# Kernel optimization log

Measured on AMD Instinct MI355X. Metric: run time of the kernel, lower is better.

The kernel has to match this reference:

```python
import jax, jax.numpy as jnp
import numpy as np
from jax import lax

CHUNK = 64
D_CONV = 4
EPS = 1e-5


def _rmsnorm(x, w):
    ms = jnp.mean(jnp.square(x.astype(jnp.float32)), axis=-1, keepdims=True)
    return x * lax.rsqrt(ms + EPS).astype(x.dtype) * w


def _conv_mix(x, proj_w, gate_w, conv_w, conv_b, out_proj_w):
    # x: [B,L,D] -> depthwise causal conv on projected channels, silu gate, out proj
    B, L, D = x.shape
    val = jnp.einsum('bld,ed->ble', x, proj_w)            # [B,L,d_inner]
    v = val.transpose(0, 2, 1)                            # [B,d_inner,L]
    d_inner = proj_w.shape[0]
    v = lax.conv_general_dilated(
        v, conv_w, window_strides=(1,), padding=[(D_CONV - 1, 0)],
        dimension_numbers=('NCH', 'OIH', 'NCH'), feature_group_count=d_inner)
    v = v + conv_b[None, :, None]
    val = jax.nn.silu(v.transpose(0, 2, 1))               # [B,L,d_inner]
    gate = jax.nn.silu(jnp.einsum('bld,ed->ble', x, gate_w))
    return jnp.einsum('ble,de->bld', val * gate, out_proj_w)


def _memory_attend(out, write_w, read_w, decay, log_alpha):
    B, T, D = out.shape
    C = CHUNK
    out32 = out.astype(jnp.float32)
    gamma = jax.nn.sigmoid(decay)
    log_gamma = jnp.log(gamma)
    v = jnp.einsum('btd,ed->bte', out32, write_w)         # proj_write
    wk = jnp.pad(out32[:, :-1], ((0, 0), (1, 0), (0, 0)))  # shifted keys
    rk = out32
    p = jnp.arange(C, dtype=jnp.float32)
    gp = gamma ** p                                       # [C]
    gw = gamma ** (C - 1 - p)                              # [C]
    diffs = jnp.maximum(p[:, None] - 1.0 - p[None, :], 0.0)
    M = jnp.exp(diffs * log_gamma) * (p[:, None] > p[None, :])  # [C,C]
    gC = gamma ** C
    Nc = T // C
    # scan axis first: [Nc,B,C,D]
    rk_c = rk.reshape(B, Nc, C, D).transpose(1, 0, 2, 3)
    wk_c = wk.reshape(B, Nc, C, D).transpose(1, 0, 2, 3)
    v_c = v.reshape(B, Nc, C, D).transpose(1, 0, 2, 3)

    def step(W, chunk):
        r, k, vv = chunk                                  # each [B,C,D]
        inter = jnp.einsum('bcd,bed->bce', r, W) * gp[None, :, None]
        S = jnp.einsum('bcd,bed->bce', r, k)              # [B,C,C]
        intra = jnp.einsum('bce,bed->bcd', S * M, vv)
        W_new = gC * W + jnp.einsum('bcd,bce->bde', vv * gw[None, :, None], k)
        return W_new, inter + intra

    W0 = jnp.zeros((B, D, D), dtype=jnp.float32)
    _, reads = lax.scan(step, W0, (rk_c, wk_c, v_c))      # [Nc,B,C,D]
    reads = reads.transpose(1, 0, 2, 3).reshape(B, T, D)
    read_out = jnp.einsum('btd,ed->bte', reads, read_w)
    return out + jnp.exp(log_alpha) * read_out.astype(out.dtype)


def setup_inputs() -> dict:
    key = jax.random.key(0)
    ks = jax.random.split(key, 9)
    B, T, D, d_inner = 8, 4096, 768, 1536
    s_d = 1.0 / np.sqrt(D)
    s_i = 1.0 / np.sqrt(d_inner)
    return {
        'x': jax.random.normal(ks[0], (B, T, D), jnp.float32),
        'norm_w': jnp.ones((D,), jnp.float32),
        'proj_w': jax.random.normal(ks[1], (d_inner, D), jnp.float32) * s_d,
        'gate_w': jax.random.normal(ks[2], (d_inner, D), jnp.float32) * s_d,
        'conv_w': jax.random.normal(ks[3], (d_inner, 1, D_CONV), jnp.float32) * 0.5,
        'conv_b': jnp.zeros((d_inner,), jnp.float32),
        'out_proj_w': jax.random.normal(ks[4], (D, d_inner), jnp.float32) * s_i,
        'write_w': jax.random.normal(ks[5], (D, D), jnp.float32) * s_d,
        'read_w': jax.random.normal(ks[6], (D, D), jnp.float32) * s_d,
        'decay': jnp.float32(4.6),
        'log_alpha': jnp.log(jnp.float32(0.03)),
    }


def reference(x, norm_w, proj_w, gate_w, conv_w, conv_b, out_proj_w, write_w, read_w, decay, log_alpha):
    out = _conv_mix(_rmsnorm(x, norm_w), proj_w, gate_w, conv_w, conv_b, out_proj_w)
    out = _memory_attend(out, write_w, read_w, decay, log_alpha)
    return x + out
```

## Files before the change

kernel.cpp:

```cpp
#include <hip/hip_runtime.h>
#include <stdint.h>


typedef short bf16s;
typedef __attribute__((ext_vector_type(8))) short short8;
typedef __attribute__((ext_vector_type(4))) float f32x4;

#define DEVINL __device__ __forceinline__

DEVINL float bf2f(short s) {
    union { unsigned u; float f; } v; v.u = ((unsigned)(unsigned short)s) << 16; return v.f;
}
DEVINL short f2bf(float f) {
    union { float f; unsigned u; } v; v.f = f;
    unsigned r = v.u + 0x7fffu + ((v.u >> 16) & 1u);
    return (short)(r >> 16);
}

DEVINL void glds16(void* lds, const void* g) {
    __builtin_amdgcn_global_load_lds(
        (const __attribute__((address_space(1))) void*)g,
        (__attribute__((address_space(3))) void*)lds, 16, 0, 0);
}

DEVINL void stage128(bf16s* lds, const bf16s* g, long gstride, int wave) {
#pragma unroll
    for (int p = 0; p < 4; ++p)
        glds16(lds + p * 2048 + wave * 512, g + (long)p * 32 * gstride);
}

DEVINL short8 fragr(const bf16s* t, int row, int kk, int q) {
    int f = kk * 4 + q;
    return *(const short8*)(t + row * 64 + ((f ^ (row & 7)) * 8));
}

#define MFMA(a, b, c) __builtin_amdgcn_mfma_f32_16x16x32_bf16((a), (b), (c), 0, 0, 0)

__global__ __launch_bounds__(256) void cast_w_kernel(
    const float* __restrict__ proj, const float* __restrict__ gate,
    const float* __restrict__ op, const float* __restrict__ wr, const float* __restrict__ rd,
    bf16s* __restrict__ w_pg, bf16s* __restrict__ w_op, bf16s* __restrict__ w_wr,
    bf16s* __restrict__ w_rd) {
    long i = (long)blockIdx.x * 256 + threadIdx.x;
    if (i < 1179648)        w_pg[i] = f2bf(proj[i]);
    else if (i < 2359296)   w_pg[i] = f2bf(gate[i - 1179648]);
    else if (i < 3538944)   w_op[i - 2359296] = f2bf(op[i - 2359296]);
    else if (i < 4128768)   w_wr[i - 3538944] = f2bf(wr[i - 3538944]);
    else if (i < 4718592)   w_rd[i - 4128768] = f2bf(rd[i - 4128768]);
}

__global__ __launch_bounds__(256) void rmsnorm_kernel(
    const float* __restrict__ x, const float* __restrict__ w, bf16s* __restrict__ xn) {
    long row = blockIdx.x;
    const float* xr = x + row * 768;
    int tid = threadIdx.x;
    float v0 = xr[tid], v1 = xr[tid + 256], v2 = xr[tid + 512];
    float ss = v0 * v0 + v1 * v1 + v2 * v2;
#pragma unroll
    for (int off = 32; off; off >>= 1) ss += __shfl_down(ss, off);
    __shared__ float p[4];
    if ((tid & 63) == 0) p[tid >> 6] = ss;
    __syncthreads();
    float tot = p[0] + p[1] + p[2] + p[3];
    float s = rsqrtf(tot * (1.0f / 768.0f) + 1e-5f);
    bf16s* o = xn + row * 768;
    o[tid]       = f2bf(v0 * s * w[tid]);
    o[tid + 256] = f2bf(v1 * s * w[tid + 256]);
    o[tid + 512] = f2bf(v2 * s * w[tid + 512]);
}

template <int MODE>
__global__ __launch_bounds__(256, 2) void gemm_kernel(
    const bf16s* __restrict__ A, const bf16s* __restrict__ B, int K, int N,
    bf16s* __restrict__ Cb, const float* __restrict__ xres,
    const bf16s* __restrict__ outres, const float* __restrict__ p_la,
    float* __restrict__ Cout) {
    __shared__ bf16s sA[128 * 64];
    __shared__ bf16s sB[128 * 64];
    const int tid = threadIdx.x;
    const int wave = tid >> 6, lane = tid & 63;
    const int wm = wave >> 1, wn = wave & 1;
    const int ln15 = lane & 15, q = lane >> 4;
    const int nbx = gridDim.x;
    const int nb = nbx * gridDim.y;
    const int l = blockIdx.y * nbx + blockIdx.x;
    const int L = (l & 7) * (nb >> 3) + (l >> 3);
    const int bx = L % nbx, by = L / nbx;
    const long m0 = (long)by * 128, n0 = (long)bx * 128;
    const int sr = tid >> 3;
    const int sf = (tid & 7) ^ (sr & 7);
    const bf16s* gA = A + (m0 + sr) * K + sf * 8;
    const bf16s* gB = B + (n0 + sr) * K + sf * 8;
    f32x4 acc[4][4] = {};
    const int nkt = K >> 6;
    for (int kt = 0; kt < nkt; ++kt) {
        __syncthreads();
        stage128(sA, gA, K, wave);
        stage128(sB, gB, K, wave);
        gA += 64; gB += 64;
        asm volatile("s_waitcnt vmcnt(0)" ::: "memory");
        __syncthreads();
#pragma unroll
        for (int kk = 0; kk < 2; ++kk) {
            short8 af[4], bf_[4];
#pragma unroll
            for (int i = 0; i < 4; ++i) af[i] = fragr(sA, wm * 64 + i * 16 + ln15, kk, q);
#pragma unroll
            for (int j = 0; j < 4; ++j) bf_[j] = fragr(sB, wn * 64 + j * 16 + ln15, kk, q);
#pragma unroll
            for (int i = 0; i < 4; ++i)
#pragma unroll
                for (int j = 0; j < 4; ++j) acc[i][j] = MFMA(af[i], bf_[j], acc[i][j]);
        }
    }
    float alpha = 0.f;
    if (MODE == 1) alpha = __expf(p_la[0]);
#pragma unroll
    for (int i = 0; i < 4; ++i)
#pragma unroll
        for (int j = 0; j < 4; ++j) {
            long mb = m0 + wm * 64 + i * 16 + q * 4;
            long nc = n0 + wn * 64 + j * 16 + ln15;
#pragma unroll
            for (int e = 0; e < 4; ++e) {
                long m = mb + e;
                float v = acc[i][j][e];
                if (MODE == 0) {
                    Cb[m * N + nc] = f2bf(v);
                } else {
                    long idx = m * 768 + nc;
                    Cout[idx] = xres[idx] + bf2f(outres[idx]) + alpha * v;
                }
            }
        }
}

__global__ __launch_bounds__(192) void conv_kernel(
    const bf16s* __restrict__ pg, const float* __restrict__ cw,
    const float* __restrict__ cb, bf16s* __restrict__ vg) {
    const int e0 = threadIdx.x * 8;
    const long l0 = (long)blockIdx.x * 16;
    float w0[8], w1[8], w2[8], w3[8], bias[8];
#pragma unroll
    for (int i = 0; i < 8; ++i) {
        const float* wc = cw + (e0 + i) * 4;
        w0[i] = wc[0]; w1[i] = wc[1]; w2[i] = wc[2]; w3[i] = wc[3];
        bias[i] = cb[e0 + i];
    }
    const bf16s* base = pg + l0 * 3072 + e0;
    short8 h0, h1, h2;
    if ((l0 & 4095) == 0) {
        short8 z = {0, 0, 0, 0, 0, 0, 0, 0};
        h0 = z; h1 = z; h2 = z;
    } else {
        h0 = *(const short8*)(base - 3 * 3072);
        h1 = *(const short8*)(base - 2 * 3072);
        h2 = *(const short8*)(base - 1 * 3072);
    }
    short8 cur = *(const short8*)base;
    short8 g8  = *(const short8*)(base + 1536);
    bf16s* out = vg + l0 * 1536 + e0;
#pragma unroll 4
    for (int t = 0; t < 16; ++t) {
        short8 ncur, ng;
        if (t < 15) {
            ncur = *(const short8*)(base + 3072);
            ng   = *(const short8*)(base + 3072 + 1536);
        }
        short8 o;
#pragma unroll
        for (int i = 0; i < 8; ++i) {
            float vv = bias[i] + bf2f(h0[i]) * w0[i] + bf2f(h1[i]) * w1[i]
                     + bf2f(h2[i]) * w2[i] + bf2f(cur[i]) * w3[i];
            float sv = vv / (1.0f + __expf(-vv));
            float gg = bf2f(g8[i]);
            o[i] = f2bf(sv * (gg / (1.0f + __expf(-gg))));
        }
        *(short8*)out = o;
        h0 = h1; h1 = h2; h2 = cur;
        cur = ncur; g8 = ng;
        base += 3072; out += 1536;
    }
}

template <int SHIFT, int GW>
__global__ __launch_bounds__(256) void transpose_kernel(
    const bf16s* __restrict__ src, bf16s* __restrict__ dst,
    const float* __restrict__ p_decay) {
    int b = blockIdx.z;
    long t0 = (long)blockIdx.y * 64, e0 = (long)blockIdx.x * 64;
    __shared__ bf16s tile[64][72];
    int tid = threadIdx.x;
    int r = tid >> 2, cs = (tid & 3) * 16;
    long tsrc = t0 + r - SHIFT;
    if (tsrc >= 0) {
        const bf16s* s = src + ((long)b * 4096 + tsrc) * 768 + e0 + cs;
        short8 v0 = *(const short8*)s;
        short8 v1 = *(const short8*)(s + 8);
        if (GW) {
            float gm = 1.0f / (1.0f + __expf(-p_decay[0]));
            float gwf = exp2f(__log2f(gm) * (float)(1023 - (int)(tsrc & 1023)));
#pragma unroll
            for (int i = 0; i < 8; ++i) {
                tile[r][cs + i]     = f2bf(bf2f(v0[i]) * gwf);
                tile[r][cs + 8 + i] = f2bf(bf2f(v1[i]) * gwf);
            }
        } else {
#pragma unroll
            for (int i = 0; i < 8; ++i) {
                tile[r][cs + i]     = v0[i];
                tile[r][cs + 8 + i] = v1[i];
            }
        }
    } else {
#pragma unroll
        for (int i = 0; i < 16; ++i) tile[r][cs + i] = 0;
    }
    __syncthreads();
    int er = tid >> 2, ts = (tid & 3) * 16;
    short8 a, bb;
#pragma unroll
    for (int i = 0; i < 8; ++i) a[i] = tile[ts + i][er];
#pragma unroll
    for (int i = 0; i < 8; ++i) bb[i] = tile[ts + 8 + i][er];
    bf16s* d = dst + ((long)b * 768 + e0 + er) * 4096 + t0 + ts;
    *(short8*)d = a;
    *(short8*)(d + 8) = bb;
}

__global__ __launch_bounds__(256, 2) void wstate_kernel(
    const bf16s* __restrict__ vTs, const bf16s* __restrict__ oTs,
    bf16s* __restrict__ Wst, const float* __restrict__ p_decay) {
    __shared__ bf16s sA[128 * 64];
    __shared__ bf16s sB[128 * 64];
    const int b = blockIdx.x;
    const int ti = blockIdx.y % 6, tj = blockIdx.y / 6;
    const int tid = threadIdx.x;
    const int wave = tid >> 6, lane = tid & 63;
    const int wm = wave >> 1, wn = wave & 1;
    const int ln15 = lane & 15, q = lane >> 4;
    const int sr = tid >> 3;
    const int sf = (tid & 7) ^ (sr & 7);
    const bf16s* gA = vTs + ((long)b * 768 + ti * 128 + sr) * 4096 + sf * 8;
    const bf16s* gB = oTs + ((long)b * 768 + tj * 128 + sr) * 4096 + sf * 8;
    const float gm = 1.0f / (1.0f + __expf(-p_decay[0]));
    const float gC = exp2f(__log2f(gm) * 1024.0f);
    f32x4 acc[4][4] = {};
    for (int jc = 0; jc < 4; ++jc) {
        bf16s* Wj = Wst + ((long)(b * 4 + jc)) * 768 * 768;
#pragma unroll
        for (int i = 0; i < 4; ++i)
#pragma unroll
            for (int jj = 0; jj < 4; ++jj) {
                long mb = ti * 128 + wm * 64 + i * 16 + q * 4;
                long nc = tj * 128 + wn * 64 + jj * 16 + ln15;
#pragma unroll
                for (int e = 0; e < 4; ++e) {
                    Wj[(mb + e) * 768 + nc] = f2bf(acc[i][jj][e]);
                    acc[i][jj][e] *= gC;
                }
            }
        for (int kt = 0; kt < 16; ++kt) {
            __syncthreads();
            stage128(sA, gA, 4096, wave);
            stage128(sB, gB, 4096, wave);
            gA += 64; gB += 64;
            asm volatile("s_waitcnt vmcnt(0)" ::: "memory");
            __syncthreads();
#pragma unroll
            for (int kk = 0; kk < 2; ++kk) {
                short8 af[4], bf_[4];
#pragma unroll
                for (int i = 0; i < 4; ++i) af[i] = fragr(sA, wm * 64 + i * 16 + ln15, kk, q);
#pragma unroll
                for (int j = 0; j < 4; ++j) bf_[j] = fragr(sB, wn * 64 + j * 16 + ln15, kk, q);
#pragma unroll
                for (int i = 0; i < 4; ++i)
#pragma unroll
                    for (int j = 0; j < 4; ++j) acc[i][j] = MFMA(af[i], bf_[j], acc[i][j]);
            }
        }
    }
}

__global__ __launch_bounds__(256, 2) void pmat_kernel(
    const bf16s* __restrict__ outb, bf16s* __restrict__ P,
    const float* __restrict__ p_decay) {
    const int b = blockIdx.x;
    const int j = blockIdx.y / 36;
    const int t = blockIdx.y % 36;
    int ci = 0;
#pragma unroll
    for (int c = 1; c < 8; ++c) ci += (c * (c + 1) / 2 <= t) ? 1 : 0;
    const int cj = t - ci * (ci + 1) / 2;
    const bool fix = (j == 0 && cj == 0);
    __shared__ bf16s sA[128 * 64];
    __shared__ bf16s sB[128 * 64];
    const int tid = threadIdx.x;
    const int wave = tid >> 6, lane = tid & 63;
    const int wm = wave >> 1, wn = wave & 1;
    const int ln15 = lane & 15, q = lane >> 4;
    const int sr = tid >> 3;
    const int sf = (tid & 7) ^ (sr & 7);
    const bf16s* gA = outb + ((long)b * 4096 + j * 1024 + ci * 128 + sr) * 768 + sf * 8;
    const bf16s* gB = outb + ((long)b * 4096 + j * 1024 + cj * 128 + sr - 1) * 768 + sf * 8;
    f32x4 acc[4][4] = {};
    for (int kt = 0; kt < 12; ++kt) {
        __syncthreads();
        stage128(sA, gA, 768, wave);
        stage128(sB, gB, 768, wave);
        gA += 64; gB += 64;
        asm volatile("s_waitcnt vmcnt(0)" ::: "memory");
        __syncthreads();
        if (fix) {
            if (tid < 8) { short8 zz = {0,0,0,0,0,0,0,0}; ((short8*)sB)[tid] = zz; }
            __syncthreads();
        }
#pragma unroll
        for (int kk = 0; kk < 2; ++kk) {
            short8 af[4], bf_[4];
#pragma unroll
            for (int i = 0; i < 4; ++i) af[i] = fragr(sA, wm * 64 + i * 16 + ln15, kk, q);
#pragma unroll
            for (int jj = 0; jj < 4; ++jj) bf_[jj] = fragr(sB, wn * 64 + jj * 16 + ln15, kk, q);
#pragma unroll
            for (int i = 0; i < 4; ++i)
#pragma unroll
                for (int jj = 0; jj < 4; ++jj) acc[i][jj] = MFMA(af[i], bf_[jj], acc[i][jj]);
        }
    }
    const float lg = __log2f(1.0f / (1.0f + __expf(-p_decay[0])));
    bf16s* Pb = P + ((long)(b * 4 + j) << 20);
#pragma unroll
    for (int i = 0; i < 4; ++i)
#pragma unroll
        for (int jj = 0; jj < 4; ++jj) {
            int cb_ = ci * 128 + wm * 64 + i * 16 + q * 4;
            int cp  = cj * 128 + wn * 64 + jj * 16 + ln15;
#pragma unroll
            for (int e = 0; e < 4; ++e) {
                int c = cb_ + e;
                float val = (c > cp) ? acc[i][jj][e] * exp2f(lg * (float)(c - 1024)) : 0.0f;
                Pb[(long)c * 1024 + cp] = f2bf(val);
            }
        }
}

__global__ __launch_bounds__(256, 2) void reads_kernel(
    const bf16s* __restrict__ outb, const bf16s* __restrict__ Wst,
    const bf16s* __restrict__ Pm, const bf16s* __restrict__ vTs,
    bf16s* __restrict__ readsb, const float* __restrict__ p_decay) {
    const int b = blockIdx.x;
    const int p = blockIdx.y / 48;
    const int inner = blockIdx.y % 48;
    const int j = (p + 1) & 3;
    const int ci = 7 - inner / 6;
    const int vi = inner % 6;
    __shared__ bf16s sA[128 * 64];
    __shared__ bf16s sB[128 * 64];
    const int tid = threadIdx.x;
    const int wave = tid >> 6, lane = tid & 63;
    const int wm = wave >> 1, wn = wave & 1;
    const int ln15 = lane & 15, q = lane >> 4;
    const int sr = tid >> 3;
    const int sf = (tid & 7) ^ (sr & 7);
    const float lg = __log2f(1.0f / (1.0f + __expf(-p_decay[0])));
    f32x4 acc[4][4] = {};
    if (j > 0) {
        const bf16s* gA = outb + ((long)b * 4096 + j * 1024 + ci * 128 + sr) * 768 + sf * 8;
        const bf16s* gB = Wst + ((long)(b * 4 + j) * 768 + vi * 128 + sr) * 768 + sf * 8;
        for (int kt = 0; kt < 12; ++kt) {
            __syncthreads();
            stage128(sA, gA, 768, wave);
            stage128(sB, gB, 768, wave);
            gA += 64; gB += 64;
            asm volatile("s_waitcnt vmcnt(0)" ::: "memory");
            __syncthreads();
#pragma unroll
            for (int kk = 0; kk < 2; ++kk) {
                short8 af[4], bf_[4];
#pragma unroll
                for (int i = 0; i < 4; ++i) af[i] = fragr(sA, wm * 64 + i * 16 + ln15, kk, q);
#pragma unroll
                for (int jj = 0; jj < 4; ++jj) bf_[jj] = fragr(sB, wn * 64 + jj * 16 + ln15, kk, q);
#pragma unroll
                for (int i = 0; i < 4; ++i)
#pragma unroll
                    for (int jj = 0; jj < 4; ++jj) acc[i][jj] = MFMA(af[i], bf_[jj], acc[i][jj]);
            }
        }
#pragma unroll
        for (int i = 0; i < 4; ++i) {
            int cb_ = ci * 128 + wm * 64 + i * 16 + q * 4;
#pragma unroll
            for (int e = 0; e < 4; ++e) {
                float s = exp2f(lg * (float)(cb_ + e));
#pragma unroll
                for (int jj = 0; jj < 4; ++jj) acc[i][jj][e] *= s;
            }
        }
    }
    {
        const bf16s* gA = Pm + ((long)(b * 4 + j) << 20) + (long)(ci * 128 + sr) * 1024 + sf * 8;
        const bf16s* gB = vTs + ((long)b * 768 + vi * 128 + sr) * 4096 + j * 1024 + sf * 8;
        const int nkt = 2 * (ci + 1);
        for (int kt = 0; kt < nkt; ++kt) {
            __syncthreads();
            stage128(sA, gA, 1024, wave);
            stage128(sB, gB, 4096, wave);
            gA += 64; gB += 64;
            asm volatile("s_waitcnt vmcnt(0)" ::: "memory");
            __syncthreads();
#pragma unroll
            for (int kk = 0; kk < 2; ++kk) {
                short8 af[4], bf_[4];
#pragma unroll
                for (int i = 0; i < 4; ++i) af[i] = fragr(sA, wm * 64 + i * 16 + ln15, kk, q);
#pragma unroll
                for (int jj = 0; jj < 4; ++jj) bf_[jj] = fragr(sB, wn * 64 + jj * 16 + ln15, kk, q);
#pragma unroll
                for (int i = 0; i < 4; ++i)
#pragma unroll
                    for (int jj = 0; jj < 4; ++jj) acc[i][jj] = MFMA(af[i], bf_[jj], acc[i][jj]);
            }
        }
    }
#pragma unroll
    for (int i = 0; i < 4; ++i)
#pragma unroll
        for (int jj = 0; jj < 4; ++jj) {
            long tb = (long)j * 1024 + ci * 128 + wm * 64 + i * 16 + q * 4;
            long nc = vi * 128 + wn * 64 + jj * 16 + ln15;
#pragma unroll
            for (int e = 0; e < 4; ++e)
                readsb[((long)b * 4096 + tb + e) * 768 + nc] = f2bf(acc[i][jj][e]);
        }
}

extern "C" void kernel_launch(void* const* d_in, const int* in_sizes, int n_in,
                              void* d_out, int out_size, void* d_ws, size_t ws_size,
                              hipStream_t stream) {
    (void)in_sizes; (void)n_in; (void)out_size;
    const float* x      = (const float*)d_in[0];
    const float* norm_w = (const float*)d_in[1];
    const float* proj_w = (const float*)d_in[2];
    const float* gate_w = (const float*)d_in[3];
    const float* conv_w = (const float*)d_in[4];
    const float* conv_b = (const float*)d_in[5];
    const float* op_w   = (const float*)d_in[6];
    const float* wr_w   = (const float*)d_in[7];
    const float* rd_w   = (const float*)d_in[8];
    const float* decay  = (const float*)d_in[9];
    const float* la     = (const float*)d_in[10];

    char* ws = (char*)d_ws;
    size_t off = 0;
    auto alloc = [&](size_t bytes) { void* p = ws + off; off += (bytes + 255) & ~(size_t)255; return p; };
    bf16s* w_pg = (bf16s*)alloc(3072l * 768 * 2);
    bf16s* w_op = (bf16s*)alloc(768l * 1536 * 2);
    bf16s* w_wr = (bf16s*)alloc(768l * 768 * 2);
    bf16s* w_rd = (bf16s*)alloc(768l * 768 * 2);
    bf16s* RA   = (bf16s*)alloc(32768l * 768 * 2);
    bf16s* RB   = (bf16s*)alloc(2 * 32768l * 768 * 2);
    bf16s* RC   = (bf16s*)alloc(2 * 32768l * 768 * 2);
    bf16s* RE   = (bf16s*)alloc(32768l * 768 * 2);
    if (ws_size < off) return;

    bf16s* xn    = RA;
    bf16s* vTs   = RA;
    bf16s* pgH   = RB;
    bf16s* vb    = RB;
    bf16s* oTs   = RB + 25165824;
    bf16s* Pm    = RB;
    bf16s* vg    = RC;
    bf16s* Wst   = RC;
    bf16s* readsb= RC + 18874368;
    bf16s* outb  = RE;

    hipLaunchKernelGGL(cast_w_kernel, dim3(18432), dim3(256), 0, stream,
                       proj_w, gate_w, op_w, wr_w, rd_w, w_pg, w_op, w_wr, w_rd);
    hipLaunchKernelGGL(rmsnorm_kernel, dim3(32768), dim3(256), 0, stream, x, norm_w, xn);
    for (int h = 0; h < 2; ++h) {
        hipLaunchKernelGGL(HIP_KERNEL_NAME(gemm_kernel<0>), dim3(24, 128), dim3(256), 0, stream,
                           xn + (long)h * 16384 * 768, w_pg, 768, 3072, pgH,
                           (const float*)nullptr, (const bf16s*)nullptr, la, (float*)nullptr);
        hipLaunchKernelGGL(conv_kernel, dim3(1024), dim3(192), 0, stream,
                           pgH, conv_w, conv_b, vg + (long)h * 16384 * 1536);
    }
    hipLaunchKernelGGL(HIP_KERNEL_NAME(gemm_kernel<0>), dim3(6, 256), dim3(256), 0, stream,
                       vg, w_op, 1536, 768, outb,
                       (const float*)nullptr, (const bf16s*)nullptr, la, (float*)nullptr);
    hipLaunchKernelGGL(HIP_KERNEL_NAME(gemm_kernel<0>), dim3(6, 256), dim3(256), 0, stream,
                       outb, w_wr, 768, 768, vb,
                       (const float*)nullptr, (const bf16s*)nullptr, la, (float*)nullptr);
    hipLaunchKernelGGL(HIP_KERNEL_NAME(transpose_kernel<1, 0>), dim3(12, 64, 8), dim3(256), 0, stream,
                       outb, oTs, decay);
    hipLaunchKernelGGL(HIP_KERNEL_NAME(transpose_kernel<0, 1>), dim3(12, 64, 8), dim3(256), 0, stream,
                       vb, vTs, decay);
    hipLaunchKernelGGL(wstate_kernel, dim3(8, 36), dim3(256), 0, stream,
                       vTs, oTs, Wst, decay);
    hipLaunchKernelGGL(pmat_kernel, dim3(8, 144), dim3(256), 0, stream,
                       outb, Pm, decay);
    hipLaunchKernelGGL(reads_kernel, dim3(8, 192), dim3(256), 0, stream,
                       outb, Wst, Pm, vTs, readsb, decay);
    hipLaunchKernelGGL(HIP_KERNEL_NAME(gemm_kernel<1>), dim3(6, 256), dim3(256), 0, stream,
                       readsb, w_rd, 768, 768, (bf16s*)nullptr,
                       x, outb, la, (float*)d_out);
}
```

Baseline: 888.5 us.

## Add pipelined 256x256 GEMM for input projection and fuse write-proj with transpose

```diff
diff --git a/kernel.cpp b/kernel.cpp
--- a/kernel.cpp
+++ b/kernel.cpp
@@ -4,6 +4,7 @@
 
 typedef short bf16s;
 typedef __attribute__((ext_vector_type(8))) short short8;
+typedef __attribute__((ext_vector_type(4))) short short4v;
 typedef __attribute__((ext_vector_type(4))) float f32x4;
 
 #define DEVINL __device__ __forceinline__
@@ -27,6 +28,12 @@
 #pragma unroll
     for (int p = 0; p < 4; ++p)
         glds16(lds + p * 2048 + wave * 512, g + (long)p * 32 * gstride);
+}
+
+DEVINL void stage_half512(bf16s* lds, const bf16s* g, long gstride, int wave) {
+#pragma unroll
+    for (int p = 0; p < 2; ++p)
+        glds16(lds + p * 4096 + wave * 512, g + (long)p * 64 * gstride);
 }
 
 DEVINL short8 fragr(const bf16s* t, int row, int kk, int q) {
@@ -74,9 +81,11 @@
     const bf16s* __restrict__ A, const bf16s* __restrict__ B, int K, int N,
     bf16s* __restrict__ Cb, const float* __restrict__ xres,
     const bf16s* __restrict__ outres, const float* __restrict__ p_la,
-    float* __restrict__ Cout) {
-    __shared__ bf16s sA[128 * 64];
-    __shared__ bf16s sB[128 * 64];
+    float* __restrict__ Cout, const float* __restrict__ p_decay,
+    bf16s* __restrict__ Tdst) {
+    __shared__ bf16s smem[128 * 136];
+    bf16s* sA = smem;
+    bf16s* sB = smem + 8192;
     const int tid = threadIdx.x;
     const int wave = tid >> 6, lane = tid & 63;
     const int wm = wave >> 1, wn = wave & 1;
@@ -113,6 +122,44 @@
                 for (int j = 0; j < 4; ++j) acc[i][j] = MFMA(af[i], bf_[j], acc[i][j]);
         }
     }
+    if (MODE == 3) {
+        __syncthreads();
+        bf16s* tbuf = smem;
+#pragma unroll
+        for (int i = 0; i < 4; ++i)
+#pragma unroll
+            for (int j = 0; j < 4; ++j) {
+                int nn = wn * 64 + j * 16 + ln15;
+                int mm = wm * 64 + i * 16 + q * 4;
+                short4v t4;
+#pragma unroll
+                for (int e = 0; e < 4; ++e) t4[e] = f2bf(acc[i][j][e]);
+                *(short4v*)(tbuf + nn * 136 + mm) = t4;
+            }
+        __syncthreads();
+        const float lg = __log2f(1.0f / (1.0f + __expf(-p_decay[0])));
+        const long b = m0 >> 12;
+        const int tb = (int)(m0 & 4095);
+#pragma unroll
+        for (int it = 0; it < 4; ++it) {
+            int chunk = it * 256 + tid;
+            int nn = chunk >> 3, mc = (chunk & 7) * 16;
+            short8 v0 = *(const short8*)(tbuf + nn * 136 + mc);
+            short8 v1 = *(const short8*)(tbuf + nn * 136 + mc + 8);
+            short8 o0, o1;
+#pragma unroll
+            for (int k2 = 0; k2 < 8; ++k2) {
+                float g0 = exp2f(lg * (float)(1023 - ((tb + mc + k2) & 1023)));
+                float g1 = exp2f(lg * (float)(1023 - ((tb + mc + 8 + k2) & 1023)));
+                o0[k2] = f2bf(bf2f(v0[k2]) * g0);
+                o1[k2] = f2bf(bf2f(v1[k2]) * g1);
+            }
+            bf16s* d = Tdst + (b * 768 + n0 + nn) * 4096 + tb + mc;
+            *(short8*)d = o0;
+            *(short8*)(d + 8) = o1;
+        }
+        return;
+    }
     float alpha = 0.f;
     if (MODE == 1) alpha = __expf(p_la[0]);
 #pragma unroll
@@ -132,6 +179,116 @@
                     Cout[idx] = xres[idx] + bf2f(outres[idx]) + alpha * v;
                 }
             }
+        }
+}
+
+#define P_MID()                                                   \
+    asm volatile("" ::: "memory");                                \
+    __builtin_amdgcn_s_barrier();                                 \
+    asm volatile("s_waitcnt lgkmcnt(0)" ::: "memory");            \
+    __builtin_amdgcn_sched_barrier(0);                            \
+    __builtin_amdgcn_s_setprio(1)
+
+#define P_END()                                                   \
+    __builtin_amdgcn_s_setprio(0);                                \
+    asm volatile("" ::: "memory");                                \
+    __builtin_amdgcn_s_barrier();                                 \
+    asm volatile("" ::: "memory")
+
+#define P_END_VM()                                                \
+    __builtin_amdgcn_s_setprio(0);                                \
+    asm volatile("s_waitcnt vmcnt(4)" ::: "memory");              \
+    asm volatile("" ::: "memory");                                \
+    __builtin_amdgcn_s_barrier();                                 \
+    asm volatile("" ::: "memory")
+
+#define RD_A(dst, s, kk)                                          \
+    _Pragma("unroll")                                             \
+    for (int m = 0; m < 8; ++m) dst[m] = fragr(&sA8[s][wm][0], m * 16 + ln15, kk, q)
+
+#define RD_B(dst, s, kk)                                          \
+    _Pragma("unroll")                                             \
+    for (int n = 0; n < 4; ++n) dst[n] = fragr(&sB8[s][bh][0], (wn & 1) * 64 + n * 16 + ln15, kk, q)
+
+#define Q_MFMA(af, bfr, nlo)                                      \
+    _Pragma("unroll")                                             \
+    for (int m = 0; m < 8; ++m) {                                 \
+        acc[m][nlo]     = MFMA(af[m], bfr[nlo],     acc[m][nlo]);     \
+        acc[m][nlo + 1] = MFMA(af[m], bfr[nlo + 1], acc[m][nlo + 1]); \
+    }
+
+__global__ __launch_bounds__(512, 2) void gemm8_kernel(
+    const bf16s* __restrict__ A, const bf16s* __restrict__ B, int K, int N,
+    bf16s* __restrict__ Cb) {
+    __shared__ bf16s sA8[2][2][8192];
+    __shared__ bf16s sB8[2][2][8192];
+    const int tid = threadIdx.x;
+    const int wave = tid >> 6, lane = tid & 63;
+    const int wm = wave >> 2, wn = wave & 3;
+    const int bh = wn >> 1;
+    const int ln15 = lane & 15, q = lane >> 4;
+    const long m0 = (long)blockIdx.y * 256, n0 = (long)blockIdx.x * 256;
+    const int sr = tid >> 3;
+    const int sf = (tid & 7) ^ (sr & 7);
+    const bf16s* pA0 = A + (m0 + sr) * K + sf * 8;
+    const bf16s* pA1 = A + (m0 + 128 + sr) * K + sf * 8;
+    const bf16s* pB0 = B + (n0 + sr) * K + sf * 8;
+    const bf16s* pB1 = B + (n0 + 128 + sr) * K + sf * 8;
+    const int NKT = K >> 6, NI = NKT >> 1;
+
+    stage_half512(&sA8[0][0][0], pA0, K, wave);
+    stage_half512(&sA8[0][1][0], pA1, K, wave);
+    stage_half512(&sB8[0][0][0], pB0, K, wave);
+    stage_half512(&sB8[0][1][0], pB1, K, wave);
+    stage_half512(&sA8[1][0][0], pA0 + 64, K, wave);
+    stage_half512(&sA8[1][1][0], pA1 + 64, K, wave);
+    asm volatile("s_waitcnt vmcnt(4)" ::: "memory");
+    asm volatile("" ::: "memory");
+    __builtin_amdgcn_s_barrier();
+    asm volatile("" ::: "memory");
+
+    f32x4 acc[8][4] = {};
+    short8 a0[8], a1[8], b0[4], b1[4];
+
+    for (int it = 0; it < NI; ++it) {
+        const long o1 = (long)(2 * it + 1) * 64;
+        int t2 = 2 * it + 2; if (t2 > NKT - 1) t2 = NKT - 1;
+        int t3 = 2 * it + 3; if (t3 > NKT - 1) t3 = NKT - 1;
+        const long o2 = (long)t2 * 64, o3 = (long)t3 * 64;
+        RD_A(a0, 0, 0); RD_B(b0, 0, 0);
+        stage_half512(&sB8[1][0][0], pB0 + o1, K, wave);
+        P_MID(); Q_MFMA(a0, b0, 0); P_END();
+        RD_A(a1, 0, 1);
+        stage_half512(&sB8[1][1][0], pB1 + o1, K, wave);
+        P_MID(); Q_MFMA(a0, b0, 2); P_END();
+        RD_B(b1, 0, 1);
+        stage_half512(&sA8[0][0][0], pA0 + o2, K, wave);
+        P_MID(); Q_MFMA(a1, b1, 0); P_END();
+        stage_half512(&sA8[0][1][0], pA1 + o2, K, wave);
+        P_MID(); Q_MFMA(a1, b1, 2); P_END_VM();
+        RD_A(a0, 1, 0); RD_B(b0, 1, 0);
+        stage_half512(&sB8[0][0][0], pB0 + o2, K, wave);
+        P_MID(); Q_MFMA(a0, b0, 0); P_END();
+        RD_A(a1, 1, 1);
+        stage_half512(&sB8[0][1][0], pB1 + o2, K, wave);
+        P_MID(); Q_MFMA(a0, b0, 2); P_END();
+        RD_B(b1, 1, 1);
+        stage_half512(&sA8[1][0][0], pA0 + o3, K, wave);
+        P_MID(); Q_MFMA(a1, b1, 0); P_END();
+        stage_half512(&sA8[1][1][0], pA1 + o3, K, wave);
+        P_MID(); Q_MFMA(a1, b1, 2); P_END_VM();
+    }
+    asm volatile("s_waitcnt vmcnt(0)" ::: "memory");
+
+#pragma unroll
+    for (int m = 0; m < 8; ++m)
+#pragma unroll
+        for (int n = 0; n < 4; ++n) {
+            long mb = m0 + wm * 128 + m * 16 + q * 4;
+            long nc = n0 + wn * 64 + n * 16 + ln15;
+#pragma unroll
+            for (int e = 0; e < 4; ++e)
+                Cb[(mb + e) * N + nc] = f2bf(acc[m][n][e]);
         }
 }
 
@@ -469,7 +626,6 @@
     bf16s* xn    = RA;
     bf16s* vTs   = RA;
     bf16s* pgH   = RB;
-    bf16s* vb    = RB;
     bf16s* oTs   = RB + 25165824;
     bf16s* Pm    = RB;
     bf16s* vg    = RC;
@@ -481,22 +637,21 @@
                        proj_w, gate_w, op_w, wr_w, rd_w, w_pg, w_op, w_wr, w_rd);
     hipLaunchKernelGGL(rmsnorm_kernel, dim3(32768), dim3(256), 0, stream, x, norm_w, xn);
     for (int h = 0; h < 2; ++h) {
-        hipLaunchKernelGGL(HIP_KERNEL_NAME(gemm_kernel<0>), dim3(24, 128), dim3(256), 0, stream,
-                           xn + (long)h * 16384 * 768, w_pg, 768, 3072, pgH,
-                           (const float*)nullptr, (const bf16s*)nullptr, la, (float*)nullptr);
+        hipLaunchKernelGGL(gemm8_kernel, dim3(12, 64), dim3(512), 0, stream,
+                           xn + (long)h * 16384 * 768, w_pg, 768, 3072, pgH);
         hipLaunchKernelGGL(conv_kernel, dim3(1024), dim3(192), 0, stream,
                            pgH, conv_w, conv_b, vg + (long)h * 16384 * 1536);
     }
     hipLaunchKernelGGL(HIP_KERNEL_NAME(gemm_kernel<0>), dim3(6, 256), dim3(256), 0, stream,
                        vg, w_op, 1536, 768, outb,
-                       (const float*)nullptr, (const bf16s*)nullptr, la, (float*)nullptr);
-    hipLaunchKernelGGL(HIP_KERNEL_NAME(gemm_kernel<0>), dim3(6, 256), dim3(256), 0, stream,
-                       outb, w_wr, 768, 768, vb,
-                       (const float*)nullptr, (const bf16s*)nullptr, la, (float*)nullptr);
+                       (const float*)nullptr, (const bf16s*)nullptr, la, (float*)nullptr,
+                       (const float*)nullptr, (bf16s*)nullptr);
+    hipLaunchKernelGGL(HIP_KERNEL_NAME(gemm_kernel<3>), dim3(6, 256), dim3(256), 0, stream,
+                       outb, w_wr, 768, 768, (bf16s*)nullptr,
+                       (const float*)nullptr, (const bf16s*)nullptr, la, (float*)nullptr,
+                       decay, vTs);
     hipLaunchKernelGGL(HIP_KERNEL_NAME(transpose_kernel<1, 0>), dim3(12, 64, 8), dim3(256), 0, stream,
                        outb, oTs, decay);
-    hipLaunchKernelGGL(HIP_KERNEL_NAME(transpose_kernel<0, 1>), dim3(12, 64, 8), dim3(256), 0, stream,
-                       vb, vTs, decay);
     hipLaunchKernelGGL(wstate_kernel, dim3(8, 36), dim3(256), 0, stream,
                        vTs, oTs, Wst, decay);
     hipLaunchKernelGGL(pmat_kernel, dim3(8, 144), dim3(256), 0, stream,
@@ -505,5 +660,6 @@
                        outb, Wst, Pm, vTs, readsb, decay);
     hipLaunchKernelGGL(HIP_KERNEL_NAME(gemm_kernel<1>), dim3(6, 256), dim3(256), 0, stream,
                        readsb, w_rd, 768, 768, (bf16s*)nullptr,
-                       x, outb, la, (float*)d_out);
-}
+                       x, outb, la, (float*)d_out,
+                       (const float*)nullptr, (bf16s*)nullptr);
+}
```

Measured after the change: 887.2 us. About the same (-0.1%).
